# Kernel tuning notes

Measured on AMD Instinct MI355X. Metric: run time of the kernel, lower is better.

The kernel has to match this reference:

```python
import jax, jax.numpy as jnp
import numpy as np

B, T, C, H = 4, 2048, 1024, 16
D = C // H


def setup_inputs() -> dict:
    key = jax.random.key(0)
    ks = jax.random.split(key, 5)
    s = C ** -0.5  # keep linear outputs O(1) like standard init
    x = jax.random.normal(ks[0], (B, T, C), dtype=jnp.float32)
    Wq = jax.random.normal(ks[1], (C, C), dtype=jnp.float32) * s
    Wk = jax.random.normal(ks[2], (C, C), dtype=jnp.float32) * s
    Wv = jax.random.normal(ks[3], (C, C), dtype=jnp.float32) * s
    Wproj = jax.random.normal(ks[4], (C, C), dtype=jnp.float32) * s
    alpha_raw = jnp.zeros((1, H, 1, 1), dtype=jnp.float32)
    beta_raw = jnp.zeros((1, H, 1, 1), dtype=jnp.float32)
    state = jnp.zeros((B, H, D, D), dtype=jnp.float32)
    return dict(x=x, Wq=Wq, Wk=Wk, Wv=Wv, Wproj=Wproj,
                alpha_raw=alpha_raw, beta_raw=beta_raw, state=state)


def reference(x, Wq, Wk, Wv, Wproj, alpha_raw, beta_raw, state):
    Bx, Tx, Cx = x.shape
    Hn = alpha_raw.shape[1]
    Dh = Cx // Hn
    # projections (torch Linear: x @ W^T), split heads -> (B, H, T, D)
    def proj(W):
        return (x @ W.T).reshape(Bx, Tx, Hn, Dh).transpose(0, 2, 1, 3)
    q, k, v = proj(Wq), proj(Wk), proj(Wv)
    # F.normalize(k, dim=-1) with eps=1e-12
    k = k / jnp.maximum(jnp.linalg.norm(k, axis=-1, keepdims=True), 1e-12)
    alpha = jax.nn.sigmoid(alpha_raw) * 0.5  # (1, H, 1, 1)
    beta = jax.nn.sigmoid(beta_raw) * 0.5

    def step(st, qkv):
        qt, kt, vt = qkv  # each (B, H, D)
        # y_t = q_t @ state^T
        y = jnp.einsum('bhe,bhde->bhd', qt, st)
        # Mk = state @ k_t
        Mk = jnp.einsum('bhde,bhe->bhd', st, kt)
        st = st - alpha * jnp.einsum('bhd,bhe->bhde', Mk, kt) \
                + beta * jnp.einsum('bhd,bhe->bhde', vt, kt)
        return st, y

    # scan over time: (T, B, H, D)
    qT = q.transpose(2, 0, 1, 3)
    kT = k.transpose(2, 0, 1, 3)
    vT = v.transpose(2, 0, 1, 3)
    state_f, ys = jax.lax.scan(step, state, (qT, kT, vT))
    y = ys.transpose(1, 0, 2, 3).reshape(Bx, Tx, Cx)  # (B, T, C)
    out = y @ Wproj.T
    return out, state_f
```

## Files before the change

kernel.cpp:

```cpp
#include <hip/hip_runtime.h>
#include <hip/hip_bf16.h>
#include <cstdint>

#define B_ 4
#define T_ 2048
#define C_ 1024
#define H_ 16
#define D_ 64
#define NC_ 32
#define L_ 64

typedef __attribute__((ext_vector_type(8))) short bf16x8;
typedef __attribute__((ext_vector_type(4))) float f32x4;

static __device__ __forceinline__ unsigned short f2bf(float f) {
  unsigned u = __float_as_uint(f);
  u += 0x7fff + ((u >> 16) & 1);
  return (unsigned short)(u >> 16);
}
static __device__ __forceinline__ float bf2f(unsigned short b) {
  return __uint_as_float(((unsigned)b) << 16);
}
static __device__ __forceinline__ int swz128(int row, int byte) {
  return row * 128 + (byte ^ ((row & 7) << 4));
}

#define LDS_BARRIER() asm volatile("s_waitcnt lgkmcnt(0)\ns_barrier" ::: "memory")

__global__ __launch_bounds__(256) void cvt_all(const float* __restrict__ x,
                                               const float* __restrict__ wq,
                                               const float* __restrict__ wk,
                                               const float* __restrict__ wv,
                                               const float* __restrict__ wp,
                                               unsigned short* __restrict__ xbf,
                                               unsigned short* __restrict__ W3,
                                               unsigned short* __restrict__ Wp) {
  const int bidx = blockIdx.x;
  const float* src;
  unsigned short* dst;
  long base;
  if (bidx < 8192) {
    src = x; dst = xbf; base = (long)bidx * 1024;
  } else {
    const int g = (bidx - 8192) >> 10;
    src = (g == 0) ? wq : (g == 1) ? wk : (g == 2) ? wv : wp;
    dst = (g < 3) ? (W3 + (long)g * 1048576) : Wp;
    base = (long)((bidx - 8192) & 1023) * 1024;
  }
  long i = base + threadIdx.x * 4;
  float4 v = *reinterpret_cast<const float4*>(src + i);
  ushort4 o;
  o.x = f2bf(v.x); o.y = f2bf(v.y); o.z = f2bf(v.z); o.w = f2bf(v.w);
  *reinterpret_cast<ushort4*>(dst + i) = o;
}


#define STAGEH(GP, GR0, KT, LOFF) do {                                            \
    const unsigned short* _s = (GP) + ((GR0) + wid * 8 + lr8) * 1024L             \
                               + (long)(KT) * 64 + skb * 8;                       \
    char* _d = (char*)lds + (LOFF) + wid * 1024;                                  \
    __builtin_amdgcn_global_load_lds((const __attribute__((address_space(1))) void*)_s,      \
        (__attribute__((address_space(3))) void*)_d, 16, 0, 0);                   \
    __builtin_amdgcn_global_load_lds((const __attribute__((address_space(1))) void*)(_s + 64 * 1024L), \
        (__attribute__((address_space(3))) void*)(_d + 8192), 16, 0, 0);          \
  } while (0)

#define PHASE1(RG, STG) do {                                                      \
    bf16x8 av[4][2], bv[4][2];                                                    \
    {                                                                             \
      const char* ab = (const char*)lds + (RG) + arow;                            \
      const char* bb = (const char*)lds + (RG) + 16384 + brow;                    \
      _Pragma("unroll")                                                           \
      for (int j = 0; j < 4; ++j) {                                               \
        av[j][0] = *(const bf16x8*)(ab + j * 4096 + cb0);                         \
        av[j][1] = *(const bf16x8*)(ab + j * 4096 + cb1);                         \
      }                                                                           \
      _Pragma("unroll")                                                           \
      for (int n = 0; n < 4; ++n) {                                               \
        bv[n][0] = *(const bf16x8*)(bb + n * 8192 + cb0);                         \
        bv[n][1] = *(const bf16x8*)(bb + n * 8192 + cb1);                         \
      }                                                                           \
    }                                                                             \
    STG;                                                                          \
    __builtin_amdgcn_s_barrier();                                                 \
    asm volatile("s_waitcnt lgkmcnt(0)" ::: "memory");                            \
    __builtin_amdgcn_sched_barrier(0);                                            \
    __builtin_amdgcn_s_setprio(1);                                                \
    _Pragma("unroll")                                                             \
    for (int j = 0; j < 4; ++j)                                                   \
      _Pragma("unroll")                                                           \
      for (int n = 0; n < 4; ++n)                                                 \
        acc[j][n] = __builtin_amdgcn_mfma_f32_16x16x32_bf16(                      \
            av[j][0], bv[n][0], acc[j][n], 0, 0, 0);                              \
    _Pragma("unroll")                                                             \
    for (int j = 0; j < 4; ++j)                                                   \
      _Pragma("unroll")                                                           \
      for (int n = 0; n < 4; ++n)                                                 \
        acc[j][n] = __builtin_amdgcn_mfma_f32_16x16x32_bf16(                      \
            av[j][1], bv[n][1], acc[j][n], 0, 0, 0);                              \
    __builtin_amdgcn_s_setprio(0);                                                \
    asm volatile("s_waitcnt vmcnt(6)" ::: "memory");                              \
    __builtin_amdgcn_s_barrier();                                                 \
  } while (0)

template<int OUT_BF16>
__global__ __launch_bounds__(512, 2) void gemm128x256(
    const unsigned short* __restrict__ A,
    const unsigned short* __restrict__ Bw,
    void* __restrict__ Cp, int N) {
  __shared__ __align__(16) char lds[147456];
  const int tid = threadIdx.x;
  const int wid = tid >> 6, lane = tid & 63;
  const int wm = wid >> 2, wn = wid & 3;
  const int f = lane & 15, g = lane >> 4;
  const int lr8 = lane >> 3, lc = lane & 7;
  const int skb = lc ^ lr8;
  const int bid = blockIdx.y * gridDim.x + blockIdx.x;
  const int cpx = (gridDim.x * gridDim.y) >> 3;
  const int sw = (bid & 7) * cpx + (bid >> 3);
  const long bM = (long)(sw / gridDim.x) * 128;
  const long bN = (long)(sw % gridDim.x) * 256;
  const int cb0 = ((0 + g) ^ (f & 7)) * 16;
  const int cb1 = ((4 + g) ^ (f & 7)) * 16;
  const int arow = (wm * 16 + f) * 128;
  const int brow = (wn * 16 + f) * 128;

  f32x4 acc[4][4] = {};

  STAGEH(Bw, bN, 0, 16384);
  STAGEH(Bw, bN + 128, 0, 32768);
  STAGEH(A, bM, 0, 0);
  STAGEH(Bw, bN, 1, 49152 + 16384);
  STAGEH(Bw, bN + 128, 1, 49152 + 32768);
  STAGEH(A, bM, 1, 49152);
  asm volatile("s_waitcnt vmcnt(6)" ::: "memory");
  __builtin_amdgcn_s_barrier();

#pragma unroll
  for (int t = 0; t < 16; ++t) {
    const int rg = (t % 3) * 49152;
    const int ng = ((t + 2) % 3) * 49152;
    const int ts = (t + 2 > 15) ? 15 : t + 2;
    PHASE1(rg,
           { STAGEH(Bw, bN, ts, ng + 16384); STAGEH(Bw, bN + 128, ts, ng + 32768); STAGEH(A, bM, ts, ng); });
  }
  asm volatile("s_waitcnt vmcnt(0)" ::: "memory");

#pragma unroll
  for (int mf = 0; mf < 4; ++mf) {
    long row = bM + mf * 32 + wm * 16 + g * 4;
#pragma unroll
    for (int nf = 0; nf < 4; ++nf) {
      long col = bN + (nf >> 1) * 128 + (nf & 1) * 64 + wn * 16 + f;
#pragma unroll
      for (int r = 0; r < 4; ++r) {
        if (OUT_BF16)
          ((unsigned short*)Cp)[(row + r) * (long)N + col] = f2bf(acc[mf][nf][r]);
        else
          ((float*)Cp)[(row + r) * (long)N + col] = acc[mf][nf][r];
      }
    }
  }
}

__global__ __launch_bounds__(256) void chunk_prep(
    unsigned short* __restrict__ qkv,
    const float* __restrict__ a_raw, const float* __restrict__ b_raw,
    unsigned short* __restrict__ Ubuf, unsigned short* __restrict__ Wbuf,
    unsigned short* __restrict__ SLbuf) {
  __shared__ __align__(16) unsigned short sK[64 * 64];
  __shared__ __align__(16) unsigned short sQ[64 * 64];
  __shared__ __align__(16) unsigned short sV[64 * 64];
  __shared__ float sA[64 * 64];

  const int blk = blockIdx.x;
  const int bh = blk >> 5, c = blk & 31;
  const int b = bh >> 4, h = bh & 15;
  const int tid = threadIdx.x;
  const int wid = tid >> 6, lane = tid & 63;

  const float alpha = 0.5f / (1.f + __expf(-a_raw[h]));
  const float beta  = 0.5f / (1.f + __expf(-b_raw[h]));

  {
    const int row = tid >> 2, cg = tid & 3;
    unsigned short* gp = qkv + (long)(b * 2048 + c * 64 + row) * 3072 + h * 64 + cg * 16;
    bf16x8 q0 = *(const bf16x8*)(gp);
    bf16x8 q1 = *(const bf16x8*)(gp + 8);
    bf16x8 k0 = *(const bf16x8*)(gp + 1024);
    bf16x8 k1 = *(const bf16x8*)(gp + 1024 + 8);
    bf16x8 v0 = *(const bf16x8*)(gp + 2048);
    bf16x8 v1 = *(const bf16x8*)(gp + 2048 + 8);
    float kf[16];
    float ss = 0.f;
#pragma unroll
    for (int i = 0; i < 8; ++i) { kf[i] = bf2f((unsigned short)k0[i]); ss += kf[i] * kf[i]; }
#pragma unroll
    for (int i = 0; i < 8; ++i) { kf[8 + i] = bf2f((unsigned short)k1[i]); ss += kf[8 + i] * kf[8 + i]; }
    ss += __shfl_xor(ss, 1);
    ss += __shfl_xor(ss, 2);
    const float inv = 1.f / fmaxf(sqrtf(ss), 1e-12f);
    bf16x8 n0, n1;
#pragma unroll
    for (int i = 0; i < 8; ++i) { n0[i] = (short)f2bf(kf[i] * inv); n1[i] = (short)f2bf(kf[8 + i] * inv); }
    *(bf16x8*)((char*)sK + swz128(row, cg * 32)) = n0;
    *(bf16x8*)((char*)sK + swz128(row, cg * 32 + 16)) = n1;
    *(bf16x8*)((char*)sQ + swz128(row, cg * 32)) = q0;
    *(bf16x8*)((char*)sQ + swz128(row, cg * 32 + 16)) = q1;
    *(bf16x8*)((char*)sV + row * 128 + cg * 32) = v0;
    *(bf16x8*)((char*)sV + row * 128 + cg * 32 + 16) = v1;
  }
  __syncthreads();

  {
    const int erow = tid >> 2, tq = tid & 3;
    unsigned short kt[16];
#pragma unroll
    for (int i = 0; i < 16; ++i)
      kt[i] = *(const unsigned short*)((const char*)sK + swz128(tq * 16 + i, 2 * erow));
    unsigned short* vp = qkv + (long)(b * 2048 + c * 64 + erow) * 3072 + 2048 + h * 64 + tq * 16;
    *(bf16x8*)vp = *(const bf16x8*)kt;
    *(bf16x8*)(vp + 8) = *(const bf16x8*)(kt + 8);
  }

  const int rfrag = lane & 15, koff = (lane >> 4) * 8, crow = (lane >> 4) * 4;
  const int w2 = wid & 1;
  if (wid < 2) {
#pragma unroll
    for (int mt = 0; mt < 2; ++mt) {
      const int m = w2 * 2 + mt;
      const int ra = 16 * m + rfrag;
      f32x4 acc[4] = {};
#pragma unroll
      for (int ks = 0; ks < 2; ++ks) {
        bf16x8 af = *(const bf16x8*)((const char*)sK + swz128(ra, ks * 64 + koff * 2));
#pragma unroll
        for (int n = 0; n < 4; ++n) {
          bf16x8 bf = *(const bf16x8*)((const char*)sK + swz128(16 * n + rfrag, ks * 64 + koff * 2));
          acc[n] = __builtin_amdgcn_mfma_f32_16x16x32_bf16(af, bf, acc[n], 0, 0, 0);
        }
      }
#pragma unroll
      for (int n = 0; n < 4; ++n)
#pragma unroll
        for (int r = 0; r < 4; ++r)
          sA[(16 * m + crow + r) * 64 + 16 * n + rfrag] = acc[n][r];
    }
  } else {
#pragma unroll
    for (int mt = 0; mt < 2; ++mt) {
      const int m = w2 * 2 + mt;
      const int ra = 16 * m + rfrag;
      f32x4 acc[4] = {};
#pragma unroll
      for (int ks = 0; ks < 2; ++ks) {
        bf16x8 af = *(const bf16x8*)((const char*)sQ + swz128(ra, ks * 64 + koff * 2));
#pragma unroll
        for (int n = 0; n < 4; ++n) {
          bf16x8 bf = *(const bf16x8*)((const char*)sK + swz128(16 * n + rfrag, ks * 64 + koff * 2));
          acc[n] = __builtin_amdgcn_mfma_f32_16x16x32_bf16(af, bf, acc[n], 0, 0, 0);
        }
      }
#pragma unroll
      for (int n = 0; n < 4; ++n)
#pragma unroll
        for (int r = 0; r < 4; ++r) {
          int t = 16 * m + crow + r, j = 16 * n + rfrag;
          SLbuf[(long)blk * 4096 + t * 64 + j] = (j < t) ? f2bf(acc[n][r]) : (unsigned short)0;
        }
    }
  }
  __syncthreads();

  if (wid < 2) {
    const int d = lane;
    float x[64];
#pragma unroll
    for (int t = 0; t < 64; ++t) {
      float rhs;
      if (wid == 0) rhs = beta * bf2f(sV[t * 64 + d]);
      else          rhs = alpha * bf2f(*(const unsigned short*)((const char*)sK + swz128(t, 2 * d)));
      float s = 0.f;
#pragma unroll
      for (int j = 0; j < t; ++j) s = fmaf(sA[t * 64 + j], x[j], s);
      x[t] = rhs - alpha * s;
    }
    unsigned short* ob = (wid == 0 ? Ubuf : Wbuf) + (long)blk * 4096 + d;
#pragma unroll
    for (int t = 0; t < 64; ++t) ob[t * 64] = f2bf(x[t]);
  }
}

__global__ __launch_bounds__(256) void chunk_scan(
    const unsigned short* __restrict__ qkv,
    const unsigned short* __restrict__ Ubuf, const unsigned short* __restrict__ Wbuf,
    const unsigned short* __restrict__ SLbuf,
    const float* __restrict__ state_in, unsigned short* __restrict__ ybuf,
    float* __restrict__ state_out) {
  __shared__ __align__(16) char lds[73728];

  const int bid0 = blockIdx.x;
  const int blk = (bid0 & 7) * 32 + (bid0 >> 3);
  const int bh = blk >> 2, dq = blk & 3;
  const int b = bh >> 4, h = bh & 15;
  const int tid = threadIdx.x, wid = tid >> 6, lane = tid & 63;
  const int rfrag = lane & 15, koff = (lane >> 4) * 8, crow = (lane >> 4) * 4;
  const int row = tid >> 2, cg = tid & 3;

  char* gt = lds + 69632;
  char* ssb = lds + 71680;

  const unsigned short* gpb = qkv + (long)(b * 2048 + row) * 3072 + h * 64 + cg * 16;
  const long tbb = ((long)(bh * 32) * 64 + row) * 64 + cg * 16;
  const long ubb = ((long)(bh * 32) * 64 + (tid >> 1)) * 64 + dq * 16 + (tid & 1) * 8;

  bf16x8 qv0, qv1, kt0, kt1, wv0, wv1, sl0, sl1, uv;
#define LOADREGS(CN) do {                                                       \
    const unsigned short* gp = gpb + (long)(CN) * 64 * 3072;                    \
    const long tb = tbb + (long)(CN) * 4096;                                    \
    qv0 = *(const bf16x8*)gp;            qv1 = *(const bf16x8*)(gp + 8);        \
    kt0 = *(const bf16x8*)(gp + 2048);   kt1 = *(const bf16x8*)(gp + 2048 + 8); \
    wv0 = *(const bf16x8*)(Wbuf + tb);   wv1 = *(const bf16x8*)(Wbuf + tb + 8); \
    sl0 = *(const bf16x8*)(SLbuf + tb);  sl1 = *(const bf16x8*)(SLbuf + tb + 8);\
    if (tid < 128) uv = *(const bf16x8*)(Ubuf + ubb + (long)(CN) * 4096);       \
  } while (0)

#define WRITE_TILES(BUF) do {                                                   \
    char* bp_ = lds + (BUF) * 34816;                                            \
    *(bf16x8*)(bp_ + swz128(row, cg * 32)) = qv0;                               \
    *(bf16x8*)(bp_ + swz128(row, cg * 32 + 16)) = qv1;                          \
    *(bf16x8*)(bp_ + 8192 + swz128(row, cg * 32)) = wv0;                        \
    *(bf16x8*)(bp_ + 8192 + swz128(row, cg * 32 + 16)) = wv1;                   \
    *(bf16x8*)(bp_ + 16384 + swz128(row, cg * 32)) = sl0;                       \
    *(bf16x8*)(bp_ + 16384 + swz128(row, cg * 32 + 16)) = sl1;                  \
    *(bf16x8*)(bp_ + 24576 + swz128(row, cg * 32)) = kt0;                       \
    *(bf16x8*)(bp_ + 24576 + swz128(row, cg * 32 + 16)) = kt1;                  \
    if (tid < 128) *(bf16x8*)(bp_ + 32768 + ((tid >> 1) * 16 + (tid & 1) * 8) * 2) = uv; \
  } while (0)

  f32x4 sacc;
#pragma unroll
  for (int r = 0; r < 4; ++r)
    sacc[r] = state_in[(long)bh * 4096 + (dq * 16 + crow + r) * 64 + 16 * wid + rfrag];
#pragma unroll
  for (int r = 0; r < 4; ++r)
    *(unsigned short*)(ssb + swz128(crow + r, 2 * (16 * wid + rfrag))) = f2bf(sacc[r]);

  LOADREGS(0);
  WRITE_TILES(0);
  LOADREGS(1);
  LDS_BARRIER();

  for (int c = 0; c < NC_; ++c) {
    const int cur = c & 1;
    const char* bp = lds + cur * 34816;
    const int ta = 16 * wid + rfrag;

    f32x4 p = {};
    f32x4 yac = {};
#pragma unroll
    for (int ks = 0; ks < 2; ++ks) {
      bf16x8 afw = *(const bf16x8*)(bp + 8192 + swz128(ta, ks * 64 + koff * 2));
      bf16x8 afq = *(const bf16x8*)(bp + swz128(ta, ks * 64 + koff * 2));
      bf16x8 bS = *(const bf16x8*)(ssb + swz128(rfrag, ks * 64 + koff * 2));
      p = __builtin_amdgcn_mfma_f32_16x16x32_bf16(afw, bS, p, 0, 0, 0);
      yac = __builtin_amdgcn_mfma_f32_16x16x32_bf16(afq, bS, yac, 0, 0, 0);
    }
#pragma unroll
    for (int r = 0; r < 4; ++r) {
      int t = 16 * wid + crow + r;
      float gg = bf2f(*(const unsigned short*)(bp + 32768 + (t * 16 + rfrag) * 2)) - p[r];
      *(unsigned short*)(gt + swz128(rfrag, 2 * t)) = f2bf(gg);
    }
    LDS_BARRIER();

#pragma unroll
    for (int ks = 0; ks < 2; ++ks) {
      bf16x8 aSL = *(const bf16x8*)(bp + 16384 + swz128(ta, ks * 64 + koff * 2));
      bf16x8 bGT = *(const bf16x8*)(gt + swz128(rfrag, ks * 64 + koff * 2));
      yac = __builtin_amdgcn_mfma_f32_16x16x32_bf16(aSL, bGT, yac, 0, 0, 0);
    }
#pragma unroll
    for (int ks = 0; ks < 2; ++ks) {
      bf16x8 aGT = *(const bf16x8*)(gt + swz128(rfrag, ks * 64 + koff * 2));
      bf16x8 bKT = *(const bf16x8*)(bp + 24576 + swz128(16 * wid + rfrag, ks * 64 + koff * 2));
      sacc = __builtin_amdgcn_mfma_f32_16x16x32_bf16(aGT, bKT, sacc, 0, 0, 0);
    }
#pragma unroll
    for (int r = 0; r < 4; ++r) {
      int t = 16 * wid + crow + r;
      ybuf[(long)(b * 2048 + c * 64 + t) * 1024 + h * 64 + dq * 16 + rfrag] = f2bf(yac[r]);
    }
#pragma unroll
    for (int r = 0; r < 4; ++r)
      *(unsigned short*)(ssb + swz128(crow + r, 2 * (16 * wid + rfrag))) = f2bf(sacc[r]);
    if (c + 1 < NC_) {
      WRITE_TILES(cur ^ 1);
      int cn = c + 2; if (cn > NC_ - 1) cn = NC_ - 1;
      LOADREGS(cn);
    }
    LDS_BARRIER();
  }

#pragma unroll
  for (int r = 0; r < 4; ++r)
    state_out[(long)bh * 4096 + (dq * 16 + crow + r) * 64 + 16 * wid + rfrag] = sacc[r];
#undef LOADREGS
#undef WRITE_TILES
}

extern "C" void kernel_launch(void* const* d_in, const int* in_sizes, int n_in,
                              void* d_out, int out_size, void* d_ws, size_t ws_size,
                              hipStream_t stream) {
  (void)in_sizes; (void)n_in; (void)out_size; (void)ws_size;
  const float* x     = (const float*)d_in[0];
  const float* Wq    = (const float*)d_in[1];
  const float* Wk    = (const float*)d_in[2];
  const float* Wv    = (const float*)d_in[3];
  const float* Wproj = (const float*)d_in[4];
  const float* a_raw = (const float*)d_in[5];
  const float* b_raw = (const float*)d_in[6];
  const float* state = (const float*)d_in[7];

  char* ws = (char*)d_ws;
  unsigned short* xbf = (unsigned short*)ws;
  unsigned short* W3  = (unsigned short*)(ws + (16l << 20));
  unsigned short* Wp  = (unsigned short*)(ws + (22l << 20));
  unsigned short* qkv = (unsigned short*)(ws + (24l << 20));
  unsigned short* Ub  = (unsigned short*)(ws + (72l << 20));
  unsigned short* Wb  = (unsigned short*)(ws + (88l << 20));
  unsigned short* SLb = (unsigned short*)(ws + (104l << 20));
  float* out = (float*)d_out;
  float* state_out = out + (long)B_ * T_ * C_;

  cvt_all<<<dim3(12288), dim3(256), 0, stream>>>(x, Wq, Wk, Wv, Wproj, xbf, W3, Wp);

  gemm128x256<1><<<dim3(3072 / 256, 8192 / 128), dim3(512), 0, stream>>>(xbf, W3, (void*)qkv, 3072);

  chunk_prep<<<dim3(2048), dim3(256), 0, stream>>>(qkv, a_raw, b_raw, Ub, Wb, SLb);
  chunk_scan<<<dim3(256), dim3(256), 0, stream>>>(qkv, Ub, Wb, SLb, state, xbf, state_out);

  gemm128x256<0><<<dim3(1024 / 256, 8192 / 128), dim3(512), 0, stream>>>(xbf, Wp, (void*)out, 1024);
}
```

Baseline: 174.1 us.

## Double-buffer GEMM register fragments and overlap LDS reads with MFMA

Reworks the bf16 128x256 GEMM main loop into a software pipeline. Each phase reads the next k-tile's A/B fragments from LDS into a second register set while the MFMAs run on the current set. Global-to-LDS prefetch is deepened to three tiles ahead. This removes the per-step stall where MFMAs waited on their own LDS reads and an extra barrier. The cost is about 32 more VGPRs for fragments under launch bounds (512,2), plus redundant clamped tail loads and reads.

```diff
diff --git a/kernel.cpp b/kernel.cpp
--- a/kernel.cpp
+++ b/kernel.cpp
@@ -65,40 +65,49 @@
         (__attribute__((address_space(3))) void*)(_d + 8192), 16, 0, 0);          \
   } while (0)
 
-#define PHASE1(RG, STG) do {                                                      \
-    bf16x8 av[4][2], bv[4][2];                                                    \
-    {                                                                             \
-      const char* ab = (const char*)lds + (RG) + arow;                            \
-      const char* bb = (const char*)lds + (RG) + 16384 + brow;                    \
-      _Pragma("unroll")                                                           \
-      for (int j = 0; j < 4; ++j) {                                               \
-        av[j][0] = *(const bf16x8*)(ab + j * 4096 + cb0);                         \
-        av[j][1] = *(const bf16x8*)(ab + j * 4096 + cb1);                         \
-      }                                                                           \
-      _Pragma("unroll")                                                           \
-      for (int n = 0; n < 4; ++n) {                                               \
-        bv[n][0] = *(const bf16x8*)(bb + n * 8192 + cb0);                         \
-        bv[n][1] = *(const bf16x8*)(bb + n * 8192 + cb1);                         \
-      }                                                                           \
+#define READF(AV, BV, RG) do {                                                    \
+    const char* ab_ = (const char*)lds + (RG) + arow;                             \
+    const char* bb_ = (const char*)lds + (RG) + 16384 + brow;                     \
+    _Pragma("unroll")                                                             \
+    for (int j = 0; j < 4; ++j) {                                                 \
+      AV[j][0] = *(const bf16x8*)(ab_ + j * 4096 + cb0);                          \
+      AV[j][1] = *(const bf16x8*)(ab_ + j * 4096 + cb1);                          \
     }                                                                             \
-    STG;                                                                          \
-    __builtin_amdgcn_s_barrier();                                                 \
-    asm volatile("s_waitcnt lgkmcnt(0)" ::: "memory");                            \
-    __builtin_amdgcn_sched_barrier(0);                                            \
-    __builtin_amdgcn_s_setprio(1);                                                \
+    _Pragma("unroll")                                                             \
+    for (int n = 0; n < 4; ++n) {                                                 \
+      BV[n][0] = *(const bf16x8*)(bb_ + n * 8192 + cb0);                          \
+      BV[n][1] = *(const bf16x8*)(bb_ + n * 8192 + cb1);                          \
+    }                                                                             \
+  } while (0)
+
+#define MFMA32(AV, BV) do {                                                       \
     _Pragma("unroll")                                                             \
     for (int j = 0; j < 4; ++j)                                                   \
       _Pragma("unroll")                                                           \
       for (int n = 0; n < 4; ++n)                                                 \
         acc[j][n] = __builtin_amdgcn_mfma_f32_16x16x32_bf16(                      \
-            av[j][0], bv[n][0], acc[j][n], 0, 0, 0);                              \
+            AV[j][0], BV[n][0], acc[j][n], 0, 0, 0);                              \
     _Pragma("unroll")                                                             \
     for (int j = 0; j < 4; ++j)                                                   \
       _Pragma("unroll")                                                           \
       for (int n = 0; n < 4; ++n)                                                 \
         acc[j][n] = __builtin_amdgcn_mfma_f32_16x16x32_bf16(                      \
-            av[j][1], bv[n][1], acc[j][n], 0, 0, 0);                              \
+            AV[j][1], BV[n][1], acc[j][n], 0, 0, 0);                              \
+  } while (0)
+
+#define PIPHASE(T, CA, CB, NA, NB) do {                                           \
+    READF(NA, NB, (((T) + 1) % 3) * 49152);                                       \
+    {                                                                             \
+      const int ts_ = ((T) + 3 > 15) ? 15 : (T) + 3;                              \
+      const int sg_ = ((T) % 3) * 49152;                                          \
+      STAGEH(Bw, bN, ts_, sg_ + 16384);                                           \
+      STAGEH(Bw, bN + 128, ts_, sg_ + 32768);                                     \
+      STAGEH(A, bM, ts_, sg_);                                                    \
+    }                                                                             \
+    __builtin_amdgcn_s_setprio(1);                                                \
+    MFMA32(CA, CB);                                                               \
     __builtin_amdgcn_s_setprio(0);                                                \
+    asm volatile("s_waitcnt lgkmcnt(0)" ::: "memory");                            \
     asm volatile("s_waitcnt vmcnt(6)" ::: "memory");                              \
     __builtin_amdgcn_s_barrier();                                                 \
   } while (0)
@@ -126,6 +135,7 @@
   const int brow = (wn * 16 + f) * 128;
 
   f32x4 acc[4][4] = {};
+  bf16x8 avA[4][2], bvA[4][2], avB[4][2], bvB[4][2];
 
   STAGEH(Bw, bN, 0, 16384);
   STAGEH(Bw, bN + 128, 0, 32768);
@@ -133,16 +143,19 @@
   STAGEH(Bw, bN, 1, 49152 + 16384);
   STAGEH(Bw, bN + 128, 1, 49152 + 32768);
   STAGEH(A, bM, 1, 49152);
+  STAGEH(Bw, bN, 2, 98304 + 16384);
+  STAGEH(Bw, bN + 128, 2, 98304 + 32768);
+  STAGEH(A, bM, 2, 98304);
   asm volatile("s_waitcnt vmcnt(6)" ::: "memory");
   __builtin_amdgcn_s_barrier();
-
-#pragma unroll
-  for (int t = 0; t < 16; ++t) {
-    const int rg = (t % 3) * 49152;
-    const int ng = ((t + 2) % 3) * 49152;
-    const int ts = (t + 2 > 15) ? 15 : t + 2;
-    PHASE1(rg,
-           { STAGEH(Bw, bN, ts, ng + 16384); STAGEH(Bw, bN + 128, ts, ng + 32768); STAGEH(A, bM, ts, ng); });
+  READF(avA, bvA, 0);
+  asm volatile("s_waitcnt lgkmcnt(0)" ::: "memory");
+  __builtin_amdgcn_s_barrier();
+
+#pragma unroll
+  for (int i = 0; i < 8; ++i) {
+    PIPHASE(2 * i,     avA, bvA, avB, bvB);
+    PIPHASE(2 * i + 1, avB, bvB, avA, bvA);
   }
   asm volatile("s_waitcnt vmcnt(0)" ::: "memory");
 
```

New measurement: 174.2 us. Within noise of the previous version (+0.1%).
